# Performance work log

Hardware: AMD Instinct MI355X
Metric: run time of the kernel (lower is better)

## Reference

```python
import jax, jax.numpy as jnp
import numpy as np

N_NODES = 50000
N_EDGES = 800000


def gcn_conv(x, edge_index, W, b):
    """PyG GCNConv: add self-loops, symmetric deg^{-1/2} normalization,
    dense transform, scatter-add aggregation."""
    n = x.shape[0]
    src, dst = edge_index[0], edge_index[1]
    # add self-loops
    loop = jnp.arange(n, dtype=src.dtype)
    src = jnp.concatenate([src, loop])
    dst = jnp.concatenate([dst, loop])
    # degree on destination nodes (includes self-loops -> deg >= 1)
    deg = jax.ops.segment_sum(jnp.ones_like(dst, dtype=x.dtype), dst, num_segments=n)
    dinv = jax.lax.rsqrt(deg)
    norm = dinv[src] * dinv[dst]  # [E+N]
    h = x @ W                     # [N, F_out] dense GEMM
    msg = h[src] * norm[:, None]  # gather + scale, [E+N, F_out]
    out = jax.ops.segment_sum(msg, dst, num_segments=n)  # scatter-add
    return out + b


def setup_inputs() -> dict:
    key = jax.random.key(0)
    ks = jax.random.split(key, 8)
    x = jax.random.normal(ks[0], (N_NODES, 100), dtype=jnp.float32)
    edge_index = jax.random.randint(ks[1], (2, N_EDGES), 0, N_NODES, dtype=jnp.int64)
    W1 = jax.random.normal(ks[2], (100, 256), dtype=jnp.float32) * 0.1
    b1 = jnp.zeros((256,), dtype=jnp.float32)
    W2 = jax.random.normal(ks[3], (256, 128), dtype=jnp.float32) * 0.06
    b2 = jnp.zeros((128,), dtype=jnp.float32)
    Wfc = jax.random.normal(ks[4], (128, 1), dtype=jnp.float32) * 0.09
    bfc = jnp.zeros((1,), dtype=jnp.float32)
    return {"x": x, "edge_index": edge_index, "W1": W1, "b1": b1,
            "W2": W2, "b2": b2, "Wfc": Wfc, "bfc": bfc}


def reference(x, edge_index, W1, b1, W2, b2, Wfc, bfc):
    # eval mode: F.dropout with training=False is identity
    h = jax.nn.relu(gcn_conv(x, edge_index, W1, b1))
    h = jax.nn.relu(gcn_conv(h, edge_index, W2, b2))
    return h @ Wfc + bfc  # [N, 1]
```

## Files before the change

### kernel.cpp

```cpp
#include <hip/hip_runtime.h>
#include <hip/hip_bf16.h>


#define F0 100
#define F1 256
#define F2 128


__global__ void zero_i32(int* p, int n) {
    int i = blockIdx.x * blockDim.x + threadIdx.x;
    if (i < n) p[i] = 0;
}

__global__ void fill_f32(float* out, const float* __restrict__ bfc, int n) {
    int i = blockIdx.x * blockDim.x + threadIdx.x;
    if (i < n) out[i] = bfc[0];
}

__global__ void deg_count_i(const int* __restrict__ dst, int* deg, int e) {
    int i = blockIdx.x * blockDim.x + threadIdx.x;
    if (i < e) atomicAdd(deg + dst[i], 1);
}

__global__ __launch_bounds__(256) void scan1(const int* __restrict__ deg,
                                             int* __restrict__ excl,
                                             int* __restrict__ bsum,
                                             float* __restrict__ dinv, int n) {
    __shared__ int wsum[4];
    int i = blockIdx.x * 256 + threadIdx.x;
    int lane = threadIdx.x & 63, wid = threadIdx.x >> 6;
    int v = (i < n) ? deg[i] : 0;
    if (i < n) dinv[i] = rsqrtf((float)(v + 1));
    int s = v;
#pragma unroll
    for (int off = 1; off < 64; off <<= 1) {
        int t = __shfl_up(s, off, 64);
        if (lane >= off) s += t;
    }
    if (lane == 63) wsum[wid] = s;
    __syncthreads();
    int add = 0;
    for (int w = 0; w < wid; w++) add += wsum[w];
    if (i < n) excl[i] = add + s - v;
    if (threadIdx.x == 255) bsum[blockIdx.x] = add + s;
}

__global__ __launch_bounds__(256) void scan2(int* __restrict__ bsum, int nb,
                                             int* __restrict__ rowptr, int n) {
    __shared__ int wsum[4];
    int lane = threadIdx.x & 63, wid = threadIdx.x >> 6;
    int v = (threadIdx.x < nb) ? bsum[threadIdx.x] : 0;
    int s = v;
#pragma unroll
    for (int off = 1; off < 64; off <<= 1) {
        int t = __shfl_up(s, off, 64);
        if (lane >= off) s += t;
    }
    if (lane == 63) wsum[wid] = s;
    __syncthreads();
    int add = 0;
    for (int w = 0; w < wid; w++) add += wsum[w];
    if (threadIdx.x < nb) bsum[threadIdx.x] = add + s - v;
    if (threadIdx.x == 255) rowptr[n] = add + s;
}

__global__ void scan3(const int* __restrict__ excl, const int* __restrict__ bsum,
                      int* __restrict__ rowptr, int* __restrict__ cursor, int n) {
    int i = blockIdx.x * 256 + threadIdx.x;
    if (i < n) {
        int r = excl[i] + bsum[blockIdx.x];
        rowptr[i] = r;
        cursor[i] = r;
    }
}

__global__ void csr_fill(const int* __restrict__ src, const int* __restrict__ dst,
                         int* cursor, int* __restrict__ csr, int e) {
    int i = blockIdx.x * blockDim.x + threadIdx.x;
    if (i < e) {
        int pos = atomicAdd(cursor + dst[i], 1);
        csr[pos] = src[i];
    }
}

__global__ void scale_x(const float4* __restrict__ x4,
                        const float* __restrict__ dinv,
                        float4* __restrict__ xs4, int n25) {
    int i = blockIdx.x * blockDim.x + threadIdx.x;
    if (i < n25) {
        float d = dinv[i / 25];
        float4 v = x4[i];
        v.x *= d; v.y *= d; v.z *= d; v.w *= d;
        xs4[i] = v;
    }
}


__global__ __launch_bounds__(256) void pull_f100(
        const float* __restrict__ xs, const int* __restrict__ rowptr,
        const int* __restrict__ csr, const float* __restrict__ dinv,
        float* __restrict__ agg, int n) {
    int wave = threadIdx.x >> 6, lane = threadIdx.x & 63;
    int v = blockIdx.x * 4 + wave;
    if (v >= n) return;
    int beg = rowptr[v], end = rowptr[v + 1];
    float dv = dinv[v];
    int half = lane >> 5, q = lane & 31;
    bool act = q < 25;
    float4 acc = {0.f, 0.f, 0.f, 0.f};
    if (half == 0 && act) acc = ((const float4*)(xs + (size_t)v * F0))[q];

    for (int base = beg; base < end; base += 64) {
        int cnt = min(64, end - base);
        int sidx = (lane < cnt) ? csr[base + lane] : 0;
        int npf = cnt >> 1;
        int p = 0;
        for (; p + 4 <= npf; p += 4) {
            int s0 = __shfl(sidx, 2 * p + half, 64);
            int s1 = __shfl(sidx, 2 * p + 2 + half, 64);
            int s2 = __shfl(sidx, 2 * p + 4 + half, 64);
            int s3 = __shfl(sidx, 2 * p + 6 + half, 64);
            if (act) {
                float4 r0 = ((const float4*)(xs + (size_t)s0 * F0))[q];
                float4 r1 = ((const float4*)(xs + (size_t)s1 * F0))[q];
                float4 r2 = ((const float4*)(xs + (size_t)s2 * F0))[q];
                float4 r3 = ((const float4*)(xs + (size_t)s3 * F0))[q];
                acc.x += (r0.x + r1.x) + (r2.x + r3.x);
                acc.y += (r0.y + r1.y) + (r2.y + r3.y);
                acc.z += (r0.z + r1.z) + (r2.z + r3.z);
                acc.w += (r0.w + r1.w) + (r2.w + r3.w);
            }
        }
        for (; p < npf; p++) {
            int s0 = __shfl(sidx, 2 * p + half, 64);
            if (act) {
                float4 r0 = ((const float4*)(xs + (size_t)s0 * F0))[q];
                acc.x += r0.x; acc.y += r0.y; acc.z += r0.z; acc.w += r0.w;
            }
        }
        if (cnt & 1) {
            int sl = __shfl(sidx, cnt - 1, 64);
            if (half == 0 && act) {
                float4 r = ((const float4*)(xs + (size_t)sl * F0))[q];
                acc.x += r.x; acc.y += r.y; acc.z += r.z; acc.w += r.w;
            }
        }
    }
    float ox = __shfl_down(acc.x, 32, 64);
    float oy = __shfl_down(acc.y, 32, 64);
    float oz = __shfl_down(acc.z, 32, 64);
    float ow = __shfl_down(acc.w, 32, 64);
    if (half == 0 && act) {
        float4 r;
        r.x = dv * (acc.x + ox);
        r.y = dv * (acc.y + oy);
        r.z = dv * (acc.z + oz);
        r.w = dv * (acc.w + ow);
        ((float4*)(agg + (size_t)v * F0))[q] = r;
    }
}

__global__ __launch_bounds__(256) void pull_c16_fused(
        const float* __restrict__ h2c, const int* __restrict__ rowptr,
        const int* __restrict__ csr, const float* __restrict__ dinv,
        const float* __restrict__ b2, const float* __restrict__ Wfc,
        float* __restrict__ out, int n) {
    int chunk = blockIdx.x & 7;
    int nb = blockIdx.x >> 3;
    int wave = threadIdx.x >> 6, lane = threadIdx.x & 63;
    int grp = lane >> 4;
    int g2  = (lane >> 2) & 3;
    int q   = lane & 3;
    int v = nb * 16 + wave * 4 + grp;
    const float* __restrict__ tab = h2c + (size_t)chunk * n * 16;

    int beg = 0, end = 0;
    float dv = 0.f;
    if (v < n) {
        beg = rowptr[v];
        end = rowptr[v + 1];
        dv = dinv[v];
    }

    float4 acc = {0.f, 0.f, 0.f, 0.f};
    if (v < n && g2 == 0) acc = ((const float4*)(tab + (size_t)v * 16))[q];

    for (int base = beg; base < end; base += 16) {
#pragma unroll
        for (int sub = 0; sub < 4; ++sub) {
            int e = base + sub * 4 + g2;
            if (e < end) {
                int s = __builtin_nontemporal_load(csr + e);
                float4 r = ((const float4*)(tab + (size_t)s * 16))[q];
                acc.x += r.x; acc.y += r.y; acc.z += r.z; acc.w += r.w;
            }
        }
    }
#pragma unroll
    for (int off = 4; off <= 8; off <<= 1) {
        acc.x += __shfl_xor(acc.x, off, 64);
        acc.y += __shfl_xor(acc.y, off, 64);
        acc.z += __shfl_xor(acc.z, off, 64);
        acc.w += __shfl_xor(acc.w, off, 64);
    }
    int c0 = chunk * 16 + 4 * q;
    float4 bb = *(const float4*)(b2 + c0);
    float4 ww = *(const float4*)(Wfc + c0);
    float part = fmaxf(fmaf(dv, acc.x, bb.x), 0.f) * ww.x
               + fmaxf(fmaf(dv, acc.y, bb.y), 0.f) * ww.y
               + fmaxf(fmaf(dv, acc.z, bb.z), 0.f) * ww.z
               + fmaxf(fmaf(dv, acc.w, bb.w), 0.f) * ww.w;
    part += __shfl_xor(part, 1, 64);
    part += __shfl_xor(part, 2, 64);
    if (v < n && (lane & 15) == 0) atomicAdd(out + v, part);
}


__global__ __launch_bounds__(256) void gemm1_tiled(
        const float* __restrict__ A, const float* __restrict__ W,
        const float* __restrict__ bias, float* __restrict__ C, int n) {
    __shared__ float As[20 * 128];
    __shared__ float Bs[20 * 128];
    int tid = threadIdx.x;
    int r0 = blockIdx.x * 128;
    int c0 = blockIdx.y * 128;
    int tc = tid & 15, tr = tid >> 4;
    float acc[8][8] = {};

    for (int k0 = 0; k0 < F0; k0 += 20) {
        if (k0) __syncthreads();
        for (int idx = tid; idx < 128 * 5; idx += 256) {
            int row = idx & 127, kq = idx >> 7;
            int gr = r0 + row;
            if (gr >= n) gr = n - 1;
            float4 v = *(const float4*)(A + (size_t)gr * F0 + k0 + 4 * kq);
            As[(4 * kq + 0) * 128 + row] = v.x;
            As[(4 * kq + 1) * 128 + row] = v.y;
            As[(4 * kq + 2) * 128 + row] = v.z;
            As[(4 * kq + 3) * 128 + row] = v.w;
        }
        for (int idx = tid; idx < 20 * 32; idx += 256) {
            int k = idx >> 5, cq = idx & 31;
            *(float4*)(Bs + k * 128 + 4 * cq) =
                *(const float4*)(W + (size_t)(k0 + k) * F1 + c0 + 4 * cq);
        }
        __syncthreads();
#pragma unroll 5
        for (int k = 0; k < 20; k++) {
            float4 a0 = *(const float4*)(As + k * 128 + 4 * tr);
            float4 a1 = *(const float4*)(As + k * 128 + 64 + 4 * tr);
            float4 b0 = *(const float4*)(Bs + k * 128 + 4 * tc);
            float4 b1 = *(const float4*)(Bs + k * 128 + 64 + 4 * tc);
            float av[8] = {a0.x, a0.y, a0.z, a0.w, a1.x, a1.y, a1.z, a1.w};
            float bv[8] = {b0.x, b0.y, b0.z, b0.w, b1.x, b1.y, b1.z, b1.w};
#pragma unroll
            for (int i = 0; i < 8; i++)
#pragma unroll
                for (int j = 0; j < 8; j++) acc[i][j] += av[i] * bv[j];
        }
    }
    float4 bb0 = *(const float4*)(bias + c0 + 4 * tc);
    float4 bb1 = *(const float4*)(bias + c0 + 64 + 4 * tc);
    float bv[8] = {bb0.x, bb0.y, bb0.z, bb0.w, bb1.x, bb1.y, bb1.z, bb1.w};
#pragma unroll
    for (int i = 0; i < 8; i++) {
        int row = (i < 4) ? (4 * tr + i) : (64 + 4 * tr + i - 4);
        int gr = r0 + row;
        if (gr < n) {
            float4 o0, o1;
            o0.x = fmaxf(acc[i][0] + bv[0], 0.f);
            o0.y = fmaxf(acc[i][1] + bv[1], 0.f);
            o0.z = fmaxf(acc[i][2] + bv[2], 0.f);
            o0.w = fmaxf(acc[i][3] + bv[3], 0.f);
            o1.x = fmaxf(acc[i][4] + bv[4], 0.f);
            o1.y = fmaxf(acc[i][5] + bv[5], 0.f);
            o1.z = fmaxf(acc[i][6] + bv[6], 0.f);
            o1.w = fmaxf(acc[i][7] + bv[7], 0.f);
            *(float4*)(C + (size_t)gr * F1 + c0 + 4 * tc) = o0;
            *(float4*)(C + (size_t)gr * F1 + c0 + 64 + 4 * tc) = o1;
        }
    }
}

__global__ __launch_bounds__(256) void gemm2_tiled(
        const float* __restrict__ A, const float* __restrict__ W,
        const float* __restrict__ dinv, float* __restrict__ C, int n) {
    __shared__ float As[32 * 128];
    __shared__ float Bs[32 * 128];
    int tid = threadIdx.x;
    int r0 = blockIdx.x * 128;
    int tc = tid & 15, tr = tid >> 4;
    float acc[8][8] = {};

    for (int k0 = 0; k0 < F1; k0 += 32) {
        if (k0) __syncthreads();
        for (int idx = tid; idx < 128 * 8; idx += 256) {
            int row = idx & 127, kq = idx >> 7;
            int gr = r0 + row;
            if (gr >= n) gr = n - 1;
            float4 v = *(const float4*)(A + (size_t)gr * F1 + k0 + 4 * kq);
            As[(4 * kq + 0) * 128 + row] = v.x;
            As[(4 * kq + 1) * 128 + row] = v.y;
            As[(4 * kq + 2) * 128 + row] = v.z;
            As[(4 * kq + 3) * 128 + row] = v.w;
        }
        for (int idx = tid; idx < 32 * 32; idx += 256) {
            int k = idx >> 5, cq = idx & 31;
            *(float4*)(Bs + k * 128 + 4 * cq) =
                *(const float4*)(W + (size_t)(k0 + k) * F2 + 4 * cq);
        }
        __syncthreads();
#pragma unroll 4
        for (int k = 0; k < 32; k++) {
            float4 a0 = *(const float4*)(As + k * 128 + 4 * tr);
            float4 a1 = *(const float4*)(As + k * 128 + 64 + 4 * tr);
            float4 b0 = *(const float4*)(Bs + k * 128 + 4 * tc);
            float4 b1 = *(const float4*)(Bs + k * 128 + 64 + 4 * tc);
            float av[8] = {a0.x, a0.y, a0.z, a0.w, a1.x, a1.y, a1.z, a1.w};
            float bv[8] = {b0.x, b0.y, b0.z, b0.w, b1.x, b1.y, b1.z, b1.w};
#pragma unroll
            for (int i = 0; i < 8; i++)
#pragma unroll
                for (int j = 0; j < 8; j++) acc[i][j] += av[i] * bv[j];
        }
    }
    int ch = tc >> 2;
    int of = (tc & 3) << 2;
#pragma unroll
    for (int i = 0; i < 8; i++) {
        int row = (i < 4) ? (4 * tr + i) : (64 + 4 * tr + i - 4);
        int gr = r0 + row;
        if (gr < n) {
            float d = dinv[gr];
            float4 o0 = {acc[i][0] * d, acc[i][1] * d, acc[i][2] * d, acc[i][3] * d};
            float4 o1 = {acc[i][4] * d, acc[i][5] * d, acc[i][6] * d, acc[i][7] * d};
            *(float4*)(C + ((size_t)ch * n + gr) * 16 + of) = o0;
            *(float4*)(C + ((size_t)(ch + 4) * n + gr) * 16 + of) = o1;
        }
    }
}


static inline size_t align16(size_t x) { return (x + 3) & ~(size_t)3; }

extern "C" void kernel_launch(void* const* d_in, const int* in_sizes, int n_in,
                              void* d_out, int out_size, void* d_ws, size_t ws_size,
                              hipStream_t stream) {
    const float* x   = (const float*)d_in[0];
    const int*   ei  = (const int*)d_in[1];
    const float* W1  = (const float*)d_in[2];
    const float* b1  = (const float*)d_in[3];
    const float* W2  = (const float*)d_in[4];
    const float* b2  = (const float*)d_in[5];
    const float* Wfc = (const float*)d_in[6];
    const float* bfc = (const float*)d_in[7];
    float* out = (float*)d_out;

    const int n = in_sizes[0] / F0;
    const int e = in_sizes[1] / 2;
    const int* src = ei;
    const int* dst = ei + e;

    char* wsb = (char*)d_ws;
    size_t off = 0;
    int* deg    = (int*)(wsb + 4 * off); off = align16(off + n);
    int* excl   = (int*)(wsb + 4 * off); off = align16(off + n);
    int* bsum   = (int*)(wsb + 4 * off); off = align16(off + 256);
    int* rowptr = (int*)(wsb + 4 * off); off = align16(off + n + 1);
    int* cursor = (int*)(wsb + 4 * off); off = align16(off + n);
    int* csr    = (int*)(wsb + 4 * off); off = align16(off + e);
    float* dinv = (float*)(wsb + 4 * off); off = align16(off + n);
    float* xs   = (float*)(wsb + 4 * off); off = align16(off + (size_t)n * F0);
    float* aggX = (float*)(wsb + 4 * off); off = align16(off + (size_t)n * F0);
    float* a1   = (float*)(wsb + 4 * off); off = align16(off + (size_t)n * F1);
    float* h2c  = (float*)(wsb + 4 * off); off = align16(off + (size_t)n * F2);

    const int B = 256;
    const int nb = (n + B - 1) / B;
    const int rblocks = (n + 127) / 128;

    zero_i32<<<nb, B, 0, stream>>>(deg, n);
    fill_f32<<<nb, B, 0, stream>>>(out, bfc, n);
    deg_count_i<<<(e + B - 1) / B, B, 0, stream>>>(dst, deg, e);
    scan1<<<nb, B, 0, stream>>>(deg, excl, bsum, dinv, n);
    scale_x<<<((n * 25) + B - 1) / B, B, 0, stream>>>(
        (const float4*)x, dinv, (float4*)xs, n * 25);
    scan2<<<1, B, 0, stream>>>(bsum, nb, rowptr, n);
    scan3<<<nb, B, 0, stream>>>(excl, bsum, rowptr, cursor, n);
    csr_fill<<<(e + B - 1) / B, B, 0, stream>>>(src, dst, cursor, csr, e);

    pull_f100<<<(n + 3) / 4, 256, 0, stream>>>(xs, rowptr, csr, dinv, aggX, n);
    gemm1_tiled<<<dim3(rblocks, F1 / 128), 256, 0, stream>>>(aggX, W1, b1, a1, n);

    gemm2_tiled<<<rblocks, 256, 0, stream>>>(a1, W2, dinv, h2c, n);
    pull_c16_fused<<<8 * ((n + 15) / 16), 256, 0, stream>>>(
        h2c, rowptr, csr, dinv, b2, Wfc, out, n);
}
```

Measured before the change: 412.7 us.

## Stage CSR neighbor indices in LDS and process 64 nodes per block in final pull

The fused second-layer aggregation now handles 64 destination nodes per block instead of 16. Each block cooperatively loads its contiguous CSR index window (in 2048-entry pieces) and row pointers into shared memory, and each 16-lane group accumulates four nodes. This is meant to replace scattered per-group global index loads with coalesced block loads and to cut the block count. The cost is extra barriers, more accumulator registers, and less parallelism per node, so high-degree nodes could leave groups unevenly loaded.

Measured after the change: 392.6 us. -4.9%, faster.

```diff
diff --git a/kernel.cpp b/kernel.cpp
--- a/kernel.cpp
+++ b/kernel.cpp
@@ -5,6 +5,7 @@
 #define F0 100
 #define F1 256
 #define F2 128
+#define CAP 2048
 
 
 __global__ void zero_i32(int* p, int n) {
@@ -165,54 +166,83 @@
         const int* __restrict__ csr, const float* __restrict__ dinv,
         const float* __restrict__ b2, const float* __restrict__ Wfc,
         float* __restrict__ out, int n) {
+    __shared__ int s_row[65];
+    __shared__ float s_dinv[64];
+    __shared__ int s_csr[CAP];
     int chunk = blockIdx.x & 7;
     int nb = blockIdx.x >> 3;
-    int wave = threadIdx.x >> 6, lane = threadIdx.x & 63;
+    int v0 = nb * 64;
+    int tid = threadIdx.x;
+    int lane = tid & 63, wv = tid >> 6;
+    int q = lane & 3;
+    int g2 = (lane >> 2) & 3;
     int grp = lane >> 4;
-    int g2  = (lane >> 2) & 3;
-    int q   = lane & 3;
-    int v = nb * 16 + wave * 4 + grp;
     const float* __restrict__ tab = h2c + (size_t)chunk * n * 16;
 
-    int beg = 0, end = 0;
-    float dv = 0.f;
-    if (v < n) {
-        beg = rowptr[v];
-        end = rowptr[v + 1];
-        dv = dinv[v];
-    }
-
-    float4 acc = {0.f, 0.f, 0.f, 0.f};
-    if (v < n && g2 == 0) acc = ((const float4*)(tab + (size_t)v * 16))[q];
-
-    for (int base = beg; base < end; base += 16) {
-#pragma unroll
-        for (int sub = 0; sub < 4; ++sub) {
-            int e = base + sub * 4 + g2;
-            if (e < end) {
-                int s = __builtin_nontemporal_load(csr + e);
+    if (tid <= 64) s_row[tid] = rowptr[min(v0 + tid, n)];
+    if (tid < 64) s_dinv[tid] = (v0 + tid < n) ? dinv[v0 + tid] : 0.f;
+    __syncthreads();
+    int ebeg = s_row[0], eend = s_row[64];
+
+    int base_local = wv * 16 + grp * 4;
+
+    float4 acc[4];
+#pragma unroll
+    for (int nn = 0; nn < 4; ++nn) acc[nn] = (float4){0.f, 0.f, 0.f, 0.f};
+
+#pragma unroll
+    for (int nn = 0; nn < 4; ++nn) {
+        int node = v0 + base_local + nn;
+        if (node < n && g2 == 0)
+            acc[nn] = ((const float4*)(tab + (size_t)node * 16))[q];
+    }
+
+    for (int w0 = ebeg; w0 < eend; w0 += CAP) {
+        int wcnt = min(CAP, eend - w0);
+        if (w0 != ebeg) __syncthreads();
+        for (int i = tid; i < wcnt; i += 256)
+            s_csr[i] = __builtin_nontemporal_load(csr + w0 + i);
+        __syncthreads();
+#pragma unroll
+        for (int nn = 0; nn < 4; ++nn) {
+            int local = base_local + nn;
+            int nbg = max(s_row[local], w0);
+            int nen = min(s_row[local + 1], w0 + wcnt);
+#pragma unroll 4
+            for (int e = nbg + g2; e < nen; e += 4) {
+                int s = s_csr[e - w0];
                 float4 r = ((const float4*)(tab + (size_t)s * 16))[q];
-                acc.x += r.x; acc.y += r.y; acc.z += r.z; acc.w += r.w;
+                acc[nn].x += r.x; acc[nn].y += r.y;
+                acc[nn].z += r.z; acc[nn].w += r.w;
             }
         }
     }
-#pragma unroll
-    for (int off = 4; off <= 8; off <<= 1) {
-        acc.x += __shfl_xor(acc.x, off, 64);
-        acc.y += __shfl_xor(acc.y, off, 64);
-        acc.z += __shfl_xor(acc.z, off, 64);
-        acc.w += __shfl_xor(acc.w, off, 64);
-    }
+
     int c0 = chunk * 16 + 4 * q;
     float4 bb = *(const float4*)(b2 + c0);
     float4 ww = *(const float4*)(Wfc + c0);
-    float part = fmaxf(fmaf(dv, acc.x, bb.x), 0.f) * ww.x
-               + fmaxf(fmaf(dv, acc.y, bb.y), 0.f) * ww.y
-               + fmaxf(fmaf(dv, acc.z, bb.z), 0.f) * ww.z
-               + fmaxf(fmaf(dv, acc.w, bb.w), 0.f) * ww.w;
-    part += __shfl_xor(part, 1, 64);
-    part += __shfl_xor(part, 2, 64);
-    if (v < n && (lane & 15) == 0) atomicAdd(out + v, part);
+#pragma unroll
+    for (int nn = 0; nn < 4; ++nn) {
+        int local = base_local + nn;
+        int node = v0 + local;
+        float dv = s_dinv[local];
+        float4 a = acc[nn];
+        a.x += __shfl_xor(a.x, 4, 64);
+        a.y += __shfl_xor(a.y, 4, 64);
+        a.z += __shfl_xor(a.z, 4, 64);
+        a.w += __shfl_xor(a.w, 4, 64);
+        a.x += __shfl_xor(a.x, 8, 64);
+        a.y += __shfl_xor(a.y, 8, 64);
+        a.z += __shfl_xor(a.z, 8, 64);
+        a.w += __shfl_xor(a.w, 8, 64);
+        float part = fmaxf(fmaf(dv, a.x, bb.x), 0.f) * ww.x
+                   + fmaxf(fmaf(dv, a.y, bb.y), 0.f) * ww.y
+                   + fmaxf(fmaf(dv, a.z, bb.z), 0.f) * ww.z
+                   + fmaxf(fmaf(dv, a.w, bb.w), 0.f) * ww.w;
+        part += __shfl_xor(part, 1, 64);
+        part += __shfl_xor(part, 2, 64);
+        if (node < n && (lane & 15) == 0) atomicAdd(out + node, part);
+    }
 }
 
 
@@ -393,6 +423,6 @@
     gemm1_tiled<<<dim3(rblocks, F1 / 128), 256, 0, stream>>>(aggX, W1, b1, a1, n);
 
     gemm2_tiled<<<rblocks, 256, 0, stream>>>(a1, W2, dinv, h2c, n);
-    pull_c16_fused<<<8 * ((n + 15) / 16), 256, 0, stream>>>(
+    pull_c16_fused<<<8 * ((n + 63) / 64), 256, 0, stream>>>(
         h2c, rowptr, csr, dinv, b2, Wfc, out, n);
 }
```
